# Kernel tuning notes

Hardware: AMD Instinct MI355X
Metric: run time of the kernel (lower is better)

The kernel has to match this reference:

```python
import jax, jax.numpy as jnp
import numpy as np

NEG_SLOPE = 0.2  # both GATConv internal LeakyReLU and the module-level activation


def gat_conv(x, src, dst, W, a_src, a_dst, bias):
    """PyG GATConv (concat=True, add_self_loops handled by caller via src/dst).
    x: [N, Din]; W: [Din, H*C]; a_src, a_dst: [H, C]; bias: [H*C]."""
    N = x.shape[0]
    H, C = a_src.shape
    h = (x @ W).reshape(N, H, C)                       # [N, H, C]
    al_src = jnp.einsum('nhc,hc->nh', h, a_src)        # [N, H]
    al_dst = jnp.einsum('nhc,hc->nh', h, a_dst)        # [N, H]
    e = jax.nn.leaky_relu(al_src[src] + al_dst[dst], NEG_SLOPE)  # [E, H]
    # segment softmax over edges grouped by destination node
    m = jax.ops.segment_max(e, dst, num_segments=N)    # [N, H]
    ex = jnp.exp(e - m[dst])
    denom = jax.ops.segment_sum(ex, dst, num_segments=N)
    alpha = ex / denom[dst]                            # [E, H]
    out = jax.ops.segment_sum(alpha[:, :, None] * h[src], dst, num_segments=N)
    return out.reshape(N, H * C) + bias


def setup_inputs() -> dict:
    key = jax.random.key(0)
    N, E = 50000, 800000
    D_IN, HID, H = 128, 128, 2
    C = HID // H
    ks = jax.random.split(key, 20)
    inp = {
        'x': jax.random.normal(ks[0], (N, D_IN), dtype=jnp.float32),
        'edge_index': jax.random.randint(ks[1], (2, E), 0, N, dtype=jnp.int64),
    }
    dims = [D_IN, HID, HID]  # input dims of the 3 GATConv layers
    for i, din in enumerate(dims, start=1):
        s = 1.0 / np.sqrt(din)
        inp[f'W{i}'] = jax.random.normal(ks[2 + 4 * i], (din, HID), dtype=jnp.float32) * s
        inp[f'a_src{i}'] = jax.random.normal(ks[3 + 4 * i], (H, C), dtype=jnp.float32) * 0.1
        inp[f'a_dst{i}'] = jax.random.normal(ks[4 + 4 * i], (H, C), dtype=jnp.float32) * 0.1
        inp[f'b{i}'] = jnp.zeros((HID,), dtype=jnp.float32)
    inp['lin_w'] = jax.random.normal(ks[2], (HID, 1), dtype=jnp.float32) * (1.0 / np.sqrt(HID))
    inp['lin_b'] = jnp.zeros((1,), dtype=jnp.float32)
    return inp


def reference(x, edge_index, W1, a_src1, a_dst1, b1, W2, a_src2, a_dst2, b2,
              W3, a_src3, a_dst3, b3, lin_w, lin_b):
    N = x.shape[0]
    loops = jnp.arange(N, dtype=edge_index.dtype)
    src = jnp.concatenate([edge_index[0], loops])  # add_self_loops=True
    dst = jnp.concatenate([edge_index[1], loops])

    h = jax.nn.leaky_relu(gat_conv(x, src, dst, W1, a_src1, a_dst1, b1), NEG_SLOPE)
    # dropout is identity in eval mode (p=0.0)
    h = jax.nn.leaky_relu(h + gat_conv(h, src, dst, W2, a_src2, a_dst2, b2), NEG_SLOPE)
    h = jax.nn.leaky_relu(h + gat_conv(h, src, dst, W3, a_src3, a_dst3, b3), NEG_SLOPE)
    logits = (h @ lin_w + lin_b).squeeze(-1)  # [N]
    return logits
```

## Files before the change

kernel.cpp:

```cpp
#include <hip/hip_runtime.h>
#include <hip/hip_bf16.h>
#include <hip/hip_fp16.h>

#define LEAK 0.2f
#define BCAP 4096
#define NTILE 8
#define TSHIFT 13

typedef _Float16 half8  __attribute__((ext_vector_type(8)));
typedef _Float16 half4v __attribute__((ext_vector_type(4)));
typedef float    float4v __attribute__((ext_vector_type(4)));


__global__ __launch_bounds__(256) void k_binscatter(const int* __restrict__ esrc,
                                                    const int* __restrict__ edst,
                                                    int* __restrict__ gcnt,
                                                    unsigned int* __restrict__ binned,
                                                    int E, int ETOT, int NBK, int eb,
                                                    const float* __restrict__ W0,
                                                    const float* __restrict__ W1,
                                                    const float* __restrict__ W2,
                                                    _Float16* __restrict__ w16t) {
    int t = threadIdx.x;
    if (blockIdx.x >= eb) {
        __shared__ _Float16 tile[64][68];
        int bb = blockIdx.x - eb;
        int m = bb >> 2;
        int ti = (bb >> 1) & 1, tj = bb & 1;
        const float* src = (m == 0) ? W0 : (m == 1 ? W1 : W2);
        _Float16* dst = w16t + m * 16384;
        for (int idx = t; idx < 4096; idx += 256) {
            int r = idx >> 6, c = idx & 63;
            tile[r][c] = (_Float16)src[(ti * 64 + r) * 128 + tj * 64 + c];
        }
        __syncthreads();
        for (int idx = t; idx < 4096; idx += 256) {
            int c = idx >> 6, r = idx & 63;
            dst[(tj * 64 + c) * 128 + ti * 64 + r] = tile[r][c];
        }
        return;
    }
    __shared__ int lh[512];
    __shared__ int lbase[512];
    for (int b = t; b < NBK; b += 256) lh[b] = 0;
    __syncthreads();
    int base = blockIdx.x * 4096;
    unsigned int word[16]; int bb[16], rk[16];
    #pragma unroll
    for (int u = 0; u < 16; ++u) {
        int e = base + u * 256 + t;
        bb[u] = -1;
        if (e < ETOT) {
            int s, d;
            if (e < E) { s = esrc[e]; d = edst[e]; } else { s = d = e - E; }
            int b = d >> 7;
            bb[u] = b;
            rk[u] = atomicAdd(&lh[b], 1);
            word[u] = (unsigned int)s | ((unsigned int)(d & 127) << 17);
        }
    }
    __syncthreads();
    for (int b = t; b < NBK; b += 256) {
        int c = lh[b];
        lbase[b] = c ? atomicAdd(&gcnt[b], c) : 0;
    }
    __syncthreads();
    #pragma unroll
    for (int u = 0; u < 16; ++u)
        if (bb[u] >= 0)
            binned[(size_t)bb[u] * BCAP + lbase[bb[u]] + rk[u]] = word[u];
}

__device__ void scatter2_body(int b, const unsigned int* __restrict__ binned,
                              const int* __restrict__ gcnt,
                              int2* __restrict__ offend,
                              int* __restrict__ csr, int N) {
    __shared__ int deg[128 * NTILE];
    __shared__ int lcur[128 * NTILE];
    __shared__ int wt[2];
    int t = threadIdx.x;
    int n0 = b << 7;
    for (int i = t; i < 128 * NTILE; i += 256) deg[i] = 0;
    __syncthreads();
    int beg = b * BCAP, end = beg + gcnt[b];
    for (int i = beg + t; i < end; i += 256) {
        unsigned int u = binned[i];
        atomicAdd(&deg[(u >> 17) * NTILE + ((u & 0x1FFFF) >> TSHIFT)], 1);
    }
    __syncthreads();
    int v = 0, x = 0;
    if (t < 128) {
        #pragma unroll
        for (int k = 0; k < NTILE; ++k) v += deg[t * NTILE + k];
        x = v;
        int lane = t & 63;
        #pragma unroll
        for (int o = 1; o < 64; o <<= 1) {
            int y = __shfl_up(x, o);
            if (lane >= o) x += y;
        }
        if (lane == 63) wt[t >> 6] = x;
    }
    __syncthreads();
    if (t < 128) {
        int excl = x - v + ((t >= 64) ? wt[0] : 0) + beg;
        int run = excl;
        #pragma unroll
        for (int k = 0; k < NTILE; ++k) {
            lcur[t * NTILE + k] = run;
            run += deg[t * NTILE + k];
        }
        int node = n0 + t;
        if (node < N) offend[node] = make_int2(excl, excl + v);
    }
    __syncthreads();
    for (int i = beg + t; i < end; i += 256) {
        unsigned int u = binned[i];
        int pos = atomicAdd(&lcur[(u >> 17) * NTILE + ((u & 0x1FFFF) >> TSHIFT)], 1);
        csr[pos] = (int)(u & 0x1FFFF);
    }
}


__global__ __launch_bounds__(256) void k_gemm_mfma(const void* __restrict__ Xv, int xfp16,
                                                   const _Float16* __restrict__ WhT,
                                                   const float* __restrict__ a_src,
                                                   const float* __restrict__ a_dst,
                                                   _Float16* __restrict__ Hout,
                                                   float* __restrict__ alsrc,
                                                   float* __restrict__ aldst, int N,
                                                   int csr_nb,
                                                   const unsigned int* __restrict__ binned,
                                                   const int* __restrict__ gcnt,
                                                   int2* __restrict__ offend,
                                                   int* __restrict__ csr) {
    if ((int)blockIdx.x < csr_nb) {
        scatter2_body((int)blockIdx.x, binned, gcnt, offend, csr, N);
        return;
    }
    __shared__ _Float16 As[64][136];
    __shared__ float sS[64][2];
    __shared__ float sD[64][2];
    const int t = threadIdx.x;
    const int lane = t & 63, w = t >> 6;
    const int block_row = ((int)blockIdx.x - csr_nb) * 64;

    if (t < 128) { sS[t >> 1][t & 1] = 0.f; sD[t >> 1][t & 1] = 0.f; }

    if (xfp16) {
        const _Float16* Xh = (const _Float16*)Xv;
        #pragma unroll
        for (int it = 0; it < 4; ++it) {
            int i = t + 256 * it;
            int row = i >> 4, c8 = i & 15;
            int gr = block_row + row;
            half8 hv = (half8){0,0,0,0,0,0,0,0};
            if (gr < N) hv = *(const half8*)(Xh + (size_t)gr * 128 + c8 * 8);
            *(half8*)(&As[row][c8 * 8]) = hv;
        }
    } else {
        const float* X = (const float*)Xv;
        #pragma unroll
        for (int it = 0; it < 8; ++it) {
            int i = t + 256 * it;
            int row = i >> 5, c4 = i & 31;
            int gr = block_row + row;
            float4 xv = make_float4(0.f, 0.f, 0.f, 0.f);
            if (gr < N) xv = *(const float4*)(X + (size_t)gr * 128 + c4 * 4);
            half4v hv;
            hv[0] = (_Float16)xv.x; hv[1] = (_Float16)xv.y;
            hv[2] = (_Float16)xv.z; hv[3] = (_Float16)xv.w;
            *(half4v*)(&As[row][c4 * 4]) = hv;
        }
    }

    const int l15 = lane & 15, kq = (lane >> 4) * 8;
    half8 bf[2][4];
    #pragma unroll
    for (int ntl = 0; ntl < 2; ++ntl) {
        int n0 = (w * 2 + ntl) * 16 + l15;
        #pragma unroll
        for (int kt = 0; kt < 4; ++kt)
            bf[ntl][kt] = *(const half8*)(WhT + (size_t)n0 * 128 + kt * 32 + kq);
    }
    __syncthreads();

    float4v acc[4][2];
    #pragma unroll
    for (int mt = 0; mt < 4; ++mt)
        #pragma unroll
        for (int ntl = 0; ntl < 2; ++ntl)
            acc[mt][ntl] = (float4v){0.f, 0.f, 0.f, 0.f};

    #pragma unroll
    for (int kt = 0; kt < 4; ++kt) {
        half8 a[4];
        #pragma unroll
        for (int mt = 0; mt < 4; ++mt)
            a[mt] = *(const half8*)(&As[mt * 16 + l15][kt * 32 + kq]);
        #pragma unroll
        for (int mt = 0; mt < 4; ++mt)
            #pragma unroll
            for (int ntl = 0; ntl < 2; ++ntl)
                acc[mt][ntl] = __builtin_amdgcn_mfma_f32_16x16x32_f16(
                    a[mt], bf[ntl][kt], acc[mt][ntl], 0, 0, 0);
    }

    #pragma unroll
    for (int mt = 0; mt < 4; ++mt) {
        int r0 = block_row + mt * 16 + (lane >> 4) * 4;
        #pragma unroll
        for (int ntl = 0; ntl < 2; ++ntl) {
            int col = (w * 2 + ntl) * 16 + l15;
            #pragma unroll
            for (int reg = 0; reg < 4; ++reg) {
                int r = r0 + reg;
                if (r < N) Hout[(size_t)r * 128 + col] = (_Float16)acc[mt][ntl][reg];
            }
        }
    }

    {
        int c0 = w * 32 + l15, c1 = c0 + 16;
        float as0 = a_src[c0], as1 = a_src[c1];
        float ad0 = a_dst[c0], ad1 = a_dst[c1];
        int head = w >> 1;
        #pragma unroll
        for (int mt = 0; mt < 4; ++mt) {
            #pragma unroll
            for (int reg = 0; reg < 4; ++reg) {
                float ps = (float)acc[mt][0][reg] * as0 + (float)acc[mt][1][reg] * as1;
                float pd = (float)acc[mt][0][reg] * ad0 + (float)acc[mt][1][reg] * ad1;
                #pragma unroll
                for (int o = 1; o < 16; o <<= 1) {
                    ps += __shfl_xor(ps, o);
                    pd += __shfl_xor(pd, o);
                }
                if (l15 == 0) {
                    int row = mt * 16 + (lane >> 4) * 4 + reg;
                    atomicAdd(&sS[row][head], ps);
                    atomicAdd(&sD[row][head], pd);
                }
            }
        }
    }
    __syncthreads();
    if (t < 128) {
        int row = t >> 1, head = t & 1;
        int gr = block_row + row;
        if (gr < N) {
            alsrc[gr * 2 + head] = sS[row][head];
            aldst[gr * 2 + head] = sD[row][head];
        }
    }
}


__global__ __launch_bounds__(256) void k_aggregate(
        const _Float16* __restrict__ H16,
        const float* __restrict__ alsrc,
        const float* __restrict__ aldst,
        const int2* __restrict__ offend,
        const int* __restrict__ csr,
        const float* __restrict__ bias,
        const _Float16* __restrict__ prev,
        _Float16* __restrict__ Out,
        const float* __restrict__ lw, const float* __restrict__ lb,
        float* __restrict__ logits, int N, int mode) {
    int wglobal = (int)((blockIdx.x * 256 + threadIdx.x) >> 6);
    int lane = threadIdx.x & 63;
    if (wglobal * 2 >= N) return;
    int half = lane >> 5;
    int hl = lane & 31;
    int node = wglobal * 2 + half;
    bool active = node < N;
    int nodeC = active ? node : (N - 1);
    int2 oe = offend[nodeC];
    int beg = oe.x;
    int end = active ? oe.y : beg;
    float2 adv = *(const float2*)(aldst + (size_t)nodeC * 2);
    float ad0 = adv.x, ad1 = adv.y;

    int p = hl & 15;
    int q = hl >> 4;
    bool head0 = p < 8;
    const _Float16* hbase = H16 + p * 8;
    int hb = half << 5;

    float acc[8];
    #pragma unroll
    for (int k = 0; k < 8; ++k) acc[k] = 0.f;
    float dsum = 0.f;

    for (int base = beg; base < end; base += 32) {
        int i = base + hl;
        int s = 0; float w0 = 0.f, w1 = 0.f;
        if (i < end) {
            s = csr[i];
            float2 al = *(const float2*)(&alsrc[s * 2]);
            float e0 = al.x + ad0; e0 = e0 > 0.f ? e0 : LEAK * e0;
            float e1 = al.y + ad1; e1 = e1 > 0.f ? e1 : LEAK * e1;
            w0 = __expf(e0); w1 = __expf(e1);
        }
        int cnt = min(32, end - base);
        int iters = (cnt + 1) >> 1;
        int jj = 0;
        for (; jj + 4 <= iters; jj += 4) {
            int sl0 = hb + (jj << 1) + q;
            int sj0 = __shfl(s, sl0), sj1 = __shfl(s, sl0 + 2);
            int sj2 = __shfl(s, sl0 + 4), sj3 = __shfl(s, sl0 + 6);
            float w00 = __shfl(w0, sl0),     w10 = __shfl(w1, sl0);
            float w01 = __shfl(w0, sl0 + 2), w11 = __shfl(w1, sl0 + 2);
            float w02 = __shfl(w0, sl0 + 4), w12 = __shfl(w1, sl0 + 4);
            float w03 = __shfl(w0, sl0 + 6), w13 = __shfl(w1, sl0 + 6);
            float ws0 = head0 ? w00 : w10;
            float ws1 = head0 ? w01 : w11;
            float ws2 = head0 ? w02 : w12;
            float ws3 = head0 ? w03 : w13;
            uint4 r0 = *(const uint4*)(hbase + (size_t)sj0 * 128);
            uint4 r1 = *(const uint4*)(hbase + (size_t)sj1 * 128);
            uint4 r2 = *(const uint4*)(hbase + (size_t)sj2 * 128);
            uint4 r3 = *(const uint4*)(hbase + (size_t)sj3 * 128);
            const _Float16* h0 = (const _Float16*)&r0;
            const _Float16* h1 = (const _Float16*)&r1;
            const _Float16* h2 = (const _Float16*)&r2;
            const _Float16* h3 = (const _Float16*)&r3;
            #pragma unroll
            for (int k = 0; k < 8; ++k) acc[k] += ws0 * (float)h0[k];
            #pragma unroll
            for (int k = 0; k < 8; ++k) acc[k] += ws1 * (float)h1[k];
            #pragma unroll
            for (int k = 0; k < 8; ++k) acc[k] += ws2 * (float)h2[k];
            #pragma unroll
            for (int k = 0; k < 8; ++k) acc[k] += ws3 * (float)h3[k];
            dsum += (ws0 + ws1) + (ws2 + ws3);
        }
        for (; jj + 2 <= iters; jj += 2) {
            int sl0 = hb + (jj << 1) + q;
            int sj0 = __shfl(s, sl0), sj1 = __shfl(s, sl0 + 2);
            float w00 = __shfl(w0, sl0),     w10 = __shfl(w1, sl0);
            float w01 = __shfl(w0, sl0 + 2), w11 = __shfl(w1, sl0 + 2);
            float ws0 = head0 ? w00 : w10;
            float ws1 = head0 ? w01 : w11;
            uint4 r0 = *(const uint4*)(hbase + (size_t)sj0 * 128);
            uint4 r1 = *(const uint4*)(hbase + (size_t)sj1 * 128);
            const _Float16* h0 = (const _Float16*)&r0;
            const _Float16* h1 = (const _Float16*)&r1;
            #pragma unroll
            for (int k = 0; k < 8; ++k) acc[k] += ws0 * (float)h0[k];
            #pragma unroll
            for (int k = 0; k < 8; ++k) acc[k] += ws1 * (float)h1[k];
            dsum += ws0 + ws1;
        }
        if (jj < iters) {
            int sl = hb + (jj << 1) + q;
            int   sj = __shfl(s,  sl);
            float wa = __shfl(w0, sl);
            float wb = __shfl(w1, sl);
            float ws = head0 ? wa : wb;
            uint4 raw = *(const uint4*)(hbase + (size_t)sj * 128);
            const _Float16* h = (const _Float16*)&raw;
            #pragma unroll
            for (int k = 0; k < 8; ++k) acc[k] += ws * (float)h[k];
            dsum += ws;
        }
    }

    #pragma unroll
    for (int k = 0; k < 8; ++k) acc[k] += __shfl_xor(acc[k], 16);
    dsum += __shfl_xor(dsum, 16);

    if (q == 0 && active) {
        float inv = 1.f / dsum;
        int c0 = p * 8;
        float v[8];
        #pragma unroll
        for (int k = 0; k < 8; ++k) v[k] = acc[k] * inv + bias[c0 + k];
        if (mode >= 1) {
            half8 pv = *(const half8*)(prev + (size_t)node * 128 + c0);
            #pragma unroll
            for (int k = 0; k < 8; ++k) v[k] += (float)pv[k];
        }
        #pragma unroll
        for (int k = 0; k < 8; ++k) v[k] = v[k] > 0.f ? v[k] : LEAK * v[k];
        if (mode == 2) {
            float partial = 0.f;
            #pragma unroll
            for (int k = 0; k < 8; ++k) partial += v[k] * lw[c0 + k];
            partial += __shfl_xor(partial, 1);
            partial += __shfl_xor(partial, 2);
            partial += __shfl_xor(partial, 4);
            partial += __shfl_xor(partial, 8);
            if (hl == 0) logits[node] = partial + lb[0];
        } else {
            half8 ov;
            #pragma unroll
            for (int k = 0; k < 8; ++k) ov[k] = (_Float16)v[k];
            *(half8*)(Out + (size_t)node * 128 + c0) = ov;
        }
    }
}


extern "C" void kernel_launch(void* const* d_in, const int* in_sizes, int n_in,
                              void* d_out, int out_size, void* d_ws, size_t ws_size,
                              hipStream_t stream) {
    const float* x    = (const float*)d_in[0];
    const int*   edge = (const int*)d_in[1];
    const float* W[3]  = {(const float*)d_in[2], (const float*)d_in[6], (const float*)d_in[10]};
    const float* as[3] = {(const float*)d_in[3], (const float*)d_in[7], (const float*)d_in[11]};
    const float* ad[3] = {(const float*)d_in[4], (const float*)d_in[8], (const float*)d_in[12]};
    const float* bs[3] = {(const float*)d_in[5], (const float*)d_in[9], (const float*)d_in[13]};
    const float* lw = (const float*)d_in[14];
    const float* lb = (const float*)d_in[15];

    const int N    = in_sizes[0] / 128;
    const int E    = in_sizes[1] / 2;
    const int ETOT = E + N;
    const int NBK  = (N + 127) >> 7;

    char* base = (char*)d_ws;
    size_t o = 0;
    auto carve = [&](size_t bytes) {
        char* p = base + o;
        o = (o + bytes + 255) & ~(size_t)255;
        return p;
    };
    int2*     offend = (int2*)    carve((size_t)N * 8);
    int*      gcnt   = (int*)     carve((size_t)NBK * 4);
    unsigned* binned = (unsigned*)carve((size_t)NBK * BCAP * 4);
    int*      csr    = (int*)     carve((size_t)NBK * BCAP * 4);
    float*    alsrc  = (float*)   carve((size_t)N * 2 * 4);
    float*    aldst  = (float*)   carve((size_t)N * 2 * 4);
    _Float16* h16    = (_Float16*)carve((size_t)N * 128 * 2);
    _Float16* bufA   = (_Float16*)carve((size_t)N * 128 * 2);
    _Float16* bufB   = (_Float16*)carve((size_t)N * 128 * 2);
    _Float16* w16t   = (_Float16*)carve((size_t)3 * 16384 * 2);
    (void)ws_size; (void)n_in; (void)out_size;

    const int* esrc = edge;
    const int* edst = edge + E;

    int eb = (ETOT + 4095) / 4096;

    hipMemsetAsync(gcnt, 0, (size_t)NBK * 4, stream);

    k_binscatter<<<eb + 12, 256, 0, stream>>>(esrc, edst, gcnt, binned, E, ETOT, NBK, eb,
                                              W[0], W[1], W[2], w16t);

    int gemm_blocks = (N + 63) / 64;
    int agg_blocks  = (N + 7) / 8;

    k_gemm_mfma<<<NBK + gemm_blocks, 256, 0, stream>>>(x, 0, w16t, as[0], ad[0], h16,
                                                       alsrc, aldst, N, NBK,
                                                       binned, gcnt, offend, csr);
    k_aggregate<<<agg_blocks, 256, 0, stream>>>(h16, alsrc, aldst, offend, csr,
                                                bs[0], nullptr, bufA, lw, lb, nullptr, N, 0);
    k_gemm_mfma<<<gemm_blocks, 256, 0, stream>>>(bufA, 1, w16t + 16384, as[1], ad[1], h16,
                                                 alsrc, aldst, N, 0,
                                                 binned, gcnt, offend, csr);
    k_aggregate<<<agg_blocks, 256, 0, stream>>>(h16, alsrc, aldst, offend, csr,
                                                bs[1], bufA, bufB, lw, lb, nullptr, N, 1);
    k_gemm_mfma<<<gemm_blocks, 256, 0, stream>>>(bufB, 1, w16t + 32768, as[2], ad[2], h16,
                                                 alsrc, aldst, N, 0,
                                                 binned, gcnt, offend, csr);
    k_aggregate<<<agg_blocks, 256, 0, stream>>>(h16, alsrc, aldst, offend, csr,
                                                bs[2], bufB, nullptr, lw, lb, (float*)d_out, N, 2);
}
```

Baseline: 269.8 us.

## Stage gathered neighbor feature rows into LDS via async global_load_lds

The aggregate kernel now bulk-gathers each chunk's neighbor rows of the fp16 feature matrix straight into LDS using global_load_lds, shared by both nodes in a wave, then reads them back from LDS in the accumulate loops. Blocks shrink to 128 threads with 32 KB of LDS per block. The aim is to issue all gathers up front and overlap their latency instead of serialising per-row register loads. In exchange it adds a full vmcnt(0) wait per chunk and LDS traffic, and the larger LDS footprint may limit occupancy.

```diff
diff --git a/kernel.cpp b/kernel.cpp
--- a/kernel.cpp
+++ b/kernel.cpp
@@ -256,7 +256,7 @@
 }
 
 
-__global__ __launch_bounds__(256) void k_aggregate(
+__global__ __launch_bounds__(128) void k_aggregate(
         const _Float16* __restrict__ H16,
         const float* __restrict__ alsrc,
         const float* __restrict__ aldst,
@@ -267,7 +267,10 @@
         _Float16* __restrict__ Out,
         const float* __restrict__ lw, const float* __restrict__ lb,
         float* __restrict__ logits, int N, int mode) {
-    int wglobal = (int)((blockIdx.x * 256 + threadIdx.x) >> 6);
+    __shared__ uint4 smem[2048];
+    int wave = threadIdx.x >> 6;
+    uint4* wvbase = smem + wave * 1024;
+    int wglobal = (int)((blockIdx.x * 128 + threadIdx.x) >> 6);
     int lane = threadIdx.x & 63;
     if (wglobal * 2 >= N) return;
     int half = lane >> 5;
@@ -284,31 +287,57 @@
     int p = hl & 15;
     int q = hl >> 4;
     bool head0 = p < 8;
-    const _Float16* hbase = H16 + p * 8;
     int hb = half << 5;
+    int g = lane >> 4;
+    int p16 = lane & 15;
+
+    int total = end - beg;
+    int tother = __shfl_xor(total, 32);
+    int maxtot = total > tother ? total : tother;
 
     float acc[8];
     #pragma unroll
     for (int k = 0; k < 8; ++k) acc[k] = 0.f;
     float dsum = 0.f;
 
-    for (int base = beg; base < end; base += 32) {
-        int i = base + hl;
+    for (int cs = 0; cs < maxtot; cs += 32) {
+        int i = beg + cs + hl;
         int s = 0; float w0 = 0.f, w1 = 0.f;
-        if (i < end) {
+        if (cs + hl < total) {
             s = csr[i];
             float2 al = *(const float2*)(&alsrc[s * 2]);
             float e0 = al.x + ad0; e0 = e0 > 0.f ? e0 : LEAK * e0;
             float e1 = al.y + ad1; e1 = e1 > 0.f ? e1 : LEAK * e1;
             w0 = __expf(e0); w1 = __expf(e1);
         }
-        int cnt = min(32, end - base);
-        int iters = (cnt + 1) >> 1;
+        int rem = total - cs;
+        int cntme = rem < 0 ? 0 : (rem > 32 ? 32 : rem);
+        int cntot = __shfl_xor(cntme, 32);
+        int c0 = half ? cntot : cntme;
+        int c1 = half ? cntme : cntot;
+        int nrows = c0 + c1;
+        if (nrows == 0) continue;
+
+        int nr1 = nrows + 1; if (nr1 > 64) nr1 = 64;
+        int nstage = (nr1 + 3) >> 2;
+        for (int k = 0; k < nstage; ++k) {
+            int m = 4 * k + g;
+            int srclane = (m < c0) ? m : (32 + m - c0);
+            srclane &= 63;
+            int sj = __shfl(s, srclane);
+            const _Float16* gp = H16 + (size_t)sj * 128 + p16 * 8;
+            __builtin_amdgcn_global_load_lds(
+                (__attribute__((address_space(1))) const void*)gp,
+                (__attribute__((address_space(3))) void*)(wvbase + k * 64),
+                16, 0, 0);
+        }
+        asm volatile("s_waitcnt vmcnt(0)" ::: "memory");
+
+        const uint4* lrow = wvbase + (size_t)((half ? c0 : 0) + q) * 16 + p;
+        int iters = (cntme + 1) >> 1;
         int jj = 0;
         for (; jj + 4 <= iters; jj += 4) {
             int sl0 = hb + (jj << 1) + q;
-            int sj0 = __shfl(s, sl0), sj1 = __shfl(s, sl0 + 2);
-            int sj2 = __shfl(s, sl0 + 4), sj3 = __shfl(s, sl0 + 6);
             float w00 = __shfl(w0, sl0),     w10 = __shfl(w1, sl0);
             float w01 = __shfl(w0, sl0 + 2), w11 = __shfl(w1, sl0 + 2);
             float w02 = __shfl(w0, sl0 + 4), w12 = __shfl(w1, sl0 + 4);
@@ -317,10 +346,10 @@
             float ws1 = head0 ? w01 : w11;
             float ws2 = head0 ? w02 : w12;
             float ws3 = head0 ? w03 : w13;
-            uint4 r0 = *(const uint4*)(hbase + (size_t)sj0 * 128);
-            uint4 r1 = *(const uint4*)(hbase + (size_t)sj1 * 128);
-            uint4 r2 = *(const uint4*)(hbase + (size_t)sj2 * 128);
-            uint4 r3 = *(const uint4*)(hbase + (size_t)sj3 * 128);
+            uint4 r0 = lrow[(jj + 0) * 32];
+            uint4 r1 = lrow[(jj + 1) * 32];
+            uint4 r2 = lrow[(jj + 2) * 32];
+            uint4 r3 = lrow[(jj + 3) * 32];
             const _Float16* h0 = (const _Float16*)&r0;
             const _Float16* h1 = (const _Float16*)&r1;
             const _Float16* h2 = (const _Float16*)&r2;
@@ -337,13 +366,12 @@
         }
         for (; jj + 2 <= iters; jj += 2) {
             int sl0 = hb + (jj << 1) + q;
-            int sj0 = __shfl(s, sl0), sj1 = __shfl(s, sl0 + 2);
             float w00 = __shfl(w0, sl0),     w10 = __shfl(w1, sl0);
             float w01 = __shfl(w0, sl0 + 2), w11 = __shfl(w1, sl0 + 2);
             float ws0 = head0 ? w00 : w10;
             float ws1 = head0 ? w01 : w11;
-            uint4 r0 = *(const uint4*)(hbase + (size_t)sj0 * 128);
-            uint4 r1 = *(const uint4*)(hbase + (size_t)sj1 * 128);
+            uint4 r0 = lrow[(jj + 0) * 32];
+            uint4 r1 = lrow[(jj + 1) * 32];
             const _Float16* h0 = (const _Float16*)&r0;
             const _Float16* h1 = (const _Float16*)&r1;
             #pragma unroll
@@ -354,11 +382,10 @@
         }
         if (jj < iters) {
             int sl = hb + (jj << 1) + q;
-            int   sj = __shfl(s,  sl);
             float wa = __shfl(w0, sl);
             float wb = __shfl(w1, sl);
             float ws = head0 ? wa : wb;
-            uint4 raw = *(const uint4*)(hbase + (size_t)sj * 128);
+            uint4 raw = lrow[jj * 32];
             const _Float16* h = (const _Float16*)&raw;
             #pragma unroll
             for (int k = 0; k < 8; ++k) acc[k] += ws * (float)h[k];
@@ -449,21 +476,21 @@
                                               W[0], W[1], W[2], w16t);
 
     int gemm_blocks = (N + 63) / 64;
-    int agg_blocks  = (N + 7) / 8;
+    int agg_blocks  = (N + 3) / 4;
 
     k_gemm_mfma<<<NBK + gemm_blocks, 256, 0, stream>>>(x, 0, w16t, as[0], ad[0], h16,
                                                        alsrc, aldst, N, NBK,
                                                        binned, gcnt, offend, csr);
-    k_aggregate<<<agg_blocks, 256, 0, stream>>>(h16, alsrc, aldst, offend, csr,
+    k_aggregate<<<agg_blocks, 128, 0, stream>>>(h16, alsrc, aldst, offend, csr,
                                                 bs[0], nullptr, bufA, lw, lb, nullptr, N, 0);
     k_gemm_mfma<<<gemm_blocks, 256, 0, stream>>>(bufA, 1, w16t + 16384, as[1], ad[1], h16,
                                                  alsrc, aldst, N, 0,
                                                  binned, gcnt, offend, csr);
-    k_aggregate<<<agg_blocks, 256, 0, stream>>>(h16, alsrc, aldst, offend, csr,
+    k_aggregate<<<agg_blocks, 128, 0, stream>>>(h16, alsrc, aldst, offend, csr,
                                                 bs[1], bufA, bufB, lw, lb, nullptr, N, 1);
     k_gemm_mfma<<<gemm_blocks, 256, 0, stream>>>(bufB, 1, w16t + 32768, as[2], ad[2], h16,
                                                  alsrc, aldst, N, 0,
                                                  binned, gcnt, offend, csr);
-    k_aggregate<<<agg_blocks, 256, 0, stream>>>(h16, alsrc, aldst, offend, csr,
+    k_aggregate<<<agg_blocks, 128, 0, stream>>>(h16, alsrc, aldst, offend, csr,
                                                 bs[2], bufB, nullptr, lw, lb, (float*)d_out, N, 2);
 }
```

After: 344.7 us. 1.28x slower.

## Fuse aggregation with next layer's GEMM and attention-logit computation

Applied to the files above, without the earlier changes.

Adds a k_agg_gemm kernel in which each 64-node block aggregates its nodes' neighbour features and writes the activated result to shared memory. It then immediately runs the next layer's MFMA GEMM and the attention-score reductions on that tile. This removes two kernel launches and the global round trip of re-reading the aggregated activations for the GEMM, at the cost of double-buffered h16 and alpha arrays. Aggregation now runs in 64-node blocks (8 nodes per wave), with a sync before the GEMM, which may lower parallelism and latency hiding in the gather phase compared with the separate aggregate kernel.

```diff
diff --git a/kernel.cpp b/kernel.cpp
--- a/kernel.cpp
+++ b/kernel.cpp
@@ -251,6 +251,235 @@
         if (gr < N) {
             alsrc[gr * 2 + head] = sS[row][head];
             aldst[gr * 2 + head] = sD[row][head];
+        }
+    }
+}
+
+
+__global__ __launch_bounds__(256) void k_agg_gemm(
+        const _Float16* __restrict__ H16in,
+        const float* __restrict__ alsrcL,
+        const float* __restrict__ aldstL,
+        const int2* __restrict__ offend,
+        const int* __restrict__ csr,
+        const float* __restrict__ biasL,
+        const _Float16* __restrict__ prev,
+        _Float16* __restrict__ Res,
+        const _Float16* __restrict__ WhT,
+        const float* __restrict__ a_src,
+        const float* __restrict__ a_dst,
+        _Float16* __restrict__ Hout,
+        float* __restrict__ alsrcO,
+        float* __restrict__ aldstO,
+        int N, int mode) {
+    __shared__ _Float16 As[64][136];
+    __shared__ float sS[64][2];
+    __shared__ float sD[64][2];
+    const int t = threadIdx.x;
+    const int lane = t & 63, w = t >> 6;
+    const int block_row = (int)blockIdx.x * 64;
+
+    if (t < 128) { sS[t >> 1][t & 1] = 0.f; sD[t >> 1][t & 1] = 0.f; }
+
+    const int half = lane >> 5;
+    const int hl = lane & 31;
+    const int p = hl & 15;
+    const int q = hl >> 4;
+    const bool head0 = p < 8;
+    const _Float16* hbase = H16in + p * 8;
+    const int hb = half << 5;
+
+    for (int j = 0; j < 8; ++j) {
+        int node = block_row + w * 16 + j * 2 + half;
+        bool active = node < N;
+        int nodeC = active ? node : (N - 1);
+        int2 oe = offend[nodeC];
+        int beg = oe.x;
+        int end = active ? oe.y : beg;
+        float2 adv = *(const float2*)(aldstL + (size_t)nodeC * 2);
+        float ad0 = adv.x, ad1 = adv.y;
+
+        float acc[8];
+        #pragma unroll
+        for (int k = 0; k < 8; ++k) acc[k] = 0.f;
+        float dsum = 0.f;
+
+        for (int base = beg; base < end; base += 32) {
+            int i = base + hl;
+            int s = 0; float w0 = 0.f, w1 = 0.f;
+            if (i < end) {
+                s = csr[i];
+                float2 al = *(const float2*)(&alsrcL[s * 2]);
+                float e0 = al.x + ad0; e0 = e0 > 0.f ? e0 : LEAK * e0;
+                float e1 = al.y + ad1; e1 = e1 > 0.f ? e1 : LEAK * e1;
+                w0 = __expf(e0); w1 = __expf(e1);
+            }
+            int cnt = min(32, end - base);
+            int iters = (cnt + 1) >> 1;
+            int jj = 0;
+            for (; jj + 4 <= iters; jj += 4) {
+                int sl0 = hb + (jj << 1) + q;
+                int sj0 = __shfl(s, sl0), sj1 = __shfl(s, sl0 + 2);
+                int sj2 = __shfl(s, sl0 + 4), sj3 = __shfl(s, sl0 + 6);
+                float w00 = __shfl(w0, sl0),     w10 = __shfl(w1, sl0);
+                float w01 = __shfl(w0, sl0 + 2), w11 = __shfl(w1, sl0 + 2);
+                float w02 = __shfl(w0, sl0 + 4), w12 = __shfl(w1, sl0 + 4);
+                float w03 = __shfl(w0, sl0 + 6), w13 = __shfl(w1, sl0 + 6);
+                float ws0 = head0 ? w00 : w10;
+                float ws1 = head0 ? w01 : w11;
+                float ws2 = head0 ? w02 : w12;
+                float ws3 = head0 ? w03 : w13;
+                uint4 r0 = *(const uint4*)(hbase + (size_t)sj0 * 128);
+                uint4 r1 = *(const uint4*)(hbase + (size_t)sj1 * 128);
+                uint4 r2 = *(const uint4*)(hbase + (size_t)sj2 * 128);
+                uint4 r3 = *(const uint4*)(hbase + (size_t)sj3 * 128);
+                const _Float16* h0 = (const _Float16*)&r0;
+                const _Float16* h1 = (const _Float16*)&r1;
+                const _Float16* h2 = (const _Float16*)&r2;
+                const _Float16* h3 = (const _Float16*)&r3;
+                #pragma unroll
+                for (int k = 0; k < 8; ++k) acc[k] += ws0 * (float)h0[k];
+                #pragma unroll
+                for (int k = 0; k < 8; ++k) acc[k] += ws1 * (float)h1[k];
+                #pragma unroll
+                for (int k = 0; k < 8; ++k) acc[k] += ws2 * (float)h2[k];
+                #pragma unroll
+                for (int k = 0; k < 8; ++k) acc[k] += ws3 * (float)h3[k];
+                dsum += (ws0 + ws1) + (ws2 + ws3);
+            }
+            for (; jj + 2 <= iters; jj += 2) {
+                int sl0 = hb + (jj << 1) + q;
+                int sj0 = __shfl(s, sl0), sj1 = __shfl(s, sl0 + 2);
+                float w00 = __shfl(w0, sl0),     w10 = __shfl(w1, sl0);
+                float w01 = __shfl(w0, sl0 + 2), w11 = __shfl(w1, sl0 + 2);
+                float ws0 = head0 ? w00 : w10;
+                float ws1 = head0 ? w01 : w11;
+                uint4 r0 = *(const uint4*)(hbase + (size_t)sj0 * 128);
+                uint4 r1 = *(const uint4*)(hbase + (size_t)sj1 * 128);
+                const _Float16* h0 = (const _Float16*)&r0;
+                const _Float16* h1 = (const _Float16*)&r1;
+                #pragma unroll
+                for (int k = 0; k < 8; ++k) acc[k] += ws0 * (float)h0[k];
+                #pragma unroll
+                for (int k = 0; k < 8; ++k) acc[k] += ws1 * (float)h1[k];
+                dsum += ws0 + ws1;
+            }
+            if (jj < iters) {
+                int sl = hb + (jj << 1) + q;
+                int   sj = __shfl(s,  sl);
+                float wa = __shfl(w0, sl);
+                float wb = __shfl(w1, sl);
+                float ws = head0 ? wa : wb;
+                uint4 raw = *(const uint4*)(hbase + (size_t)sj * 128);
+                const _Float16* h = (const _Float16*)&raw;
+                #pragma unroll
+                for (int k = 0; k < 8; ++k) acc[k] += ws * (float)h[k];
+                dsum += ws;
+            }
+        }
+
+        #pragma unroll
+        for (int k = 0; k < 8; ++k) acc[k] += __shfl_xor(acc[k], 16);
+        dsum += __shfl_xor(dsum, 16);
+
+        if (q == 0 && active) {
+            float inv = 1.f / dsum;
+            int c0 = p * 8;
+            float v[8];
+            #pragma unroll
+            for (int k = 0; k < 8; ++k) v[k] = acc[k] * inv + biasL[c0 + k];
+            if (mode >= 1) {
+                half8 pv = *(const half8*)(prev + (size_t)node * 128 + c0);
+                #pragma unroll
+                for (int k = 0; k < 8; ++k) v[k] += (float)pv[k];
+            }
+            #pragma unroll
+            for (int k = 0; k < 8; ++k) v[k] = v[k] > 0.f ? v[k] : LEAK * v[k];
+            half8 ov;
+            #pragma unroll
+            for (int k = 0; k < 8; ++k) ov[k] = (_Float16)v[k];
+            *(half8*)(&As[node - block_row][c0]) = ov;
+            *(half8*)(Res + (size_t)node * 128 + c0) = ov;
+        }
+    }
+    __syncthreads();
+
+    const int l15 = lane & 15, kq = (lane >> 4) * 8;
+    half8 bf[2][4];
+    #pragma unroll
+    for (int ntl = 0; ntl < 2; ++ntl) {
+        int n0 = (w * 2 + ntl) * 16 + l15;
+        #pragma unroll
+        for (int kt = 0; kt < 4; ++kt)
+            bf[ntl][kt] = *(const half8*)(WhT + (size_t)n0 * 128 + kt * 32 + kq);
+    }
+
+    float4v accB[4][2];
+    #pragma unroll
+    for (int mt = 0; mt < 4; ++mt)
+        #pragma unroll
+        for (int ntl = 0; ntl < 2; ++ntl)
+            accB[mt][ntl] = (float4v){0.f, 0.f, 0.f, 0.f};
+
+    #pragma unroll
+    for (int kt = 0; kt < 4; ++kt) {
+        half8 a[4];
+        #pragma unroll
+        for (int mt = 0; mt < 4; ++mt)
+            a[mt] = *(const half8*)(&As[mt * 16 + l15][kt * 32 + kq]);
+        #pragma unroll
+        for (int mt = 0; mt < 4; ++mt)
+            #pragma unroll
+            for (int ntl = 0; ntl < 2; ++ntl)
+                accB[mt][ntl] = __builtin_amdgcn_mfma_f32_16x16x32_f16(
+                    a[mt], bf[ntl][kt], accB[mt][ntl], 0, 0, 0);
+    }
+
+    #pragma unroll
+    for (int mt = 0; mt < 4; ++mt) {
+        int r0 = block_row + mt * 16 + (lane >> 4) * 4;
+        #pragma unroll
+        for (int ntl = 0; ntl < 2; ++ntl) {
+            int col = (w * 2 + ntl) * 16 + l15;
+            #pragma unroll
+            for (int reg = 0; reg < 4; ++reg) {
+                int r = r0 + reg;
+                if (r < N) Hout[(size_t)r * 128 + col] = (_Float16)accB[mt][ntl][reg];
+            }
+        }
+    }
+
+    {
+        int c0 = w * 32 + l15, c1 = c0 + 16;
+        float as0 = a_src[c0], as1 = a_src[c1];
+        float ad0 = a_dst[c0], ad1 = a_dst[c1];
+        int head = w >> 1;
+        #pragma unroll
+        for (int mt = 0; mt < 4; ++mt) {
+            #pragma unroll
+            for (int reg = 0; reg < 4; ++reg) {
+                float ps = (float)accB[mt][0][reg] * as0 + (float)accB[mt][1][reg] * as1;
+                float pd = (float)accB[mt][0][reg] * ad0 + (float)accB[mt][1][reg] * ad1;
+                #pragma unroll
+                for (int o = 1; o < 16; o <<= 1) {
+                    ps += __shfl_xor(ps, o);
+                    pd += __shfl_xor(pd, o);
+                }
+                if (l15 == 0) {
+                    int row = mt * 16 + (lane >> 4) * 4 + reg;
+                    atomicAdd(&sS[row][head], ps);
+                    atomicAdd(&sD[row][head], pd);
+                }
+            }
+        }
+    }
+    __syncthreads();
+    if (t < 128) {
+        int row = t >> 1, head = t & 1;
+        int gr = block_row + row;
+        if (gr < N) {
+            alsrcO[gr * 2 + head] = sS[row][head];
+            aldstO[gr * 2 + head] = sD[row][head];
         }
     }
 }
@@ -430,9 +659,12 @@
     int*      gcnt   = (int*)     carve((size_t)NBK * 4);
     unsigned* binned = (unsigned*)carve((size_t)NBK * BCAP * 4);
     int*      csr    = (int*)     carve((size_t)NBK * BCAP * 4);
-    float*    alsrc  = (float*)   carve((size_t)N * 2 * 4);
-    float*    aldst  = (float*)   carve((size_t)N * 2 * 4);
-    _Float16* h16    = (_Float16*)carve((size_t)N * 128 * 2);
+    float*    alsA   = (float*)   carve((size_t)N * 2 * 4);
+    float*    aldA   = (float*)   carve((size_t)N * 2 * 4);
+    float*    alsB   = (float*)   carve((size_t)N * 2 * 4);
+    float*    aldB   = (float*)   carve((size_t)N * 2 * 4);
+    _Float16* h16a   = (_Float16*)carve((size_t)N * 128 * 2);
+    _Float16* h16b   = (_Float16*)carve((size_t)N * 128 * 2);
     _Float16* bufA   = (_Float16*)carve((size_t)N * 128 * 2);
     _Float16* bufB   = (_Float16*)carve((size_t)N * 128 * 2);
     _Float16* w16t   = (_Float16*)carve((size_t)3 * 16384 * 2);
@@ -451,19 +683,18 @@
     int gemm_blocks = (N + 63) / 64;
     int agg_blocks  = (N + 7) / 8;
 
-    k_gemm_mfma<<<NBK + gemm_blocks, 256, 0, stream>>>(x, 0, w16t, as[0], ad[0], h16,
-                                                       alsrc, aldst, N, NBK,
+    k_gemm_mfma<<<NBK + gemm_blocks, 256, 0, stream>>>(x, 0, w16t, as[0], ad[0], h16a,
+                                                       alsA, aldA, N, NBK,
                                                        binned, gcnt, offend, csr);
-    k_aggregate<<<agg_blocks, 256, 0, stream>>>(h16, alsrc, aldst, offend, csr,
-                                                bs[0], nullptr, bufA, lw, lb, nullptr, N, 0);
-    k_gemm_mfma<<<gemm_blocks, 256, 0, stream>>>(bufA, 1, w16t + 16384, as[1], ad[1], h16,
-                                                 alsrc, aldst, N, 0,
-                                                 binned, gcnt, offend, csr);
-    k_aggregate<<<agg_blocks, 256, 0, stream>>>(h16, alsrc, aldst, offend, csr,
-                                                bs[1], bufA, bufB, lw, lb, nullptr, N, 1);
-    k_gemm_mfma<<<gemm_blocks, 256, 0, stream>>>(bufB, 1, w16t + 32768, as[2], ad[2], h16,
-                                                 alsrc, aldst, N, 0,
-                                                 binned, gcnt, offend, csr);
-    k_aggregate<<<agg_blocks, 256, 0, stream>>>(h16, alsrc, aldst, offend, csr,
-                                                bs[2], bufB, nullptr, lw, lb, (float*)d_out, N, 2);
+    k_agg_gemm<<<gemm_blocks, 256, 0, stream>>>(h16a, alsA, aldA, offend, csr,
+                                                bs[0], nullptr, bufA,
+                                                w16t + 16384, as[1], ad[1],
+                                                h16b, alsB, aldB, N, 0);
+    k_agg_gemm<<<gemm_blocks, 256, 0, stream>>>(h16b, alsB, aldB, offend, csr,
+                                                bs[1], bufA, bufB,
+                                                w16t + 32768, as[2], ad[2],
+                                                h16a, alsA, aldA, N, 1);
+    k_aggregate<<<agg_blocks, 256, 0, stream>>>(h16a, alsA, aldA, offend, csr,
+                                                bs[2], bufB, nullptr, lw, lb,
+                                                (float*)d_out, N, 2);
 }
```

Result: no change. 264.5 us (-1.9%).

## Split aggregation by attention head with XCD-aware block mapping

Applied to the files above, without the earlier changes.

The aggregation kernel now gives each block a single attention head. The head and a node subgroup come from the block ID's low three bits, so each XCD works on one head's 64-column half of H16, which should improve L2 locality on the multi-die GPU. Each 16-lane group handles one node for one head, so the two-head shuffle-and-select logic goes away. The final linear layer now combines the two heads' partial logits with atomicAdd, which needs logits zeroed beforehand; that zeroing is done inside the binscatter kernel. The cost is twice as many node visits, each with its own edge-list and CSR reads, plus atomics on the output.

```diff
diff --git a/kernel.cpp b/kernel.cpp
--- a/kernel.cpp
+++ b/kernel.cpp
@@ -20,7 +20,8 @@
                                                     const float* __restrict__ W0,
                                                     const float* __restrict__ W1,
                                                     const float* __restrict__ W2,
-                                                    _Float16* __restrict__ w16t) {
+                                                    _Float16* __restrict__ w16t,
+                                                    float* __restrict__ logits, int N) {
     int t = threadIdx.x;
     if (blockIdx.x >= eb) {
         __shared__ _Float16 tile[64][68];
@@ -38,6 +39,7 @@
             int c = idx >> 6, r = idx & 63;
             dst[(tj * 64 + c) * 128 + ti * 64 + r] = tile[r][c];
         }
+        for (int i = bb * 256 + t; i < N; i += 12 * 256) logits[i] = 0.f;
         return;
     }
     __shared__ int lh[512];
@@ -256,7 +258,7 @@
 }
 
 
-__global__ __launch_bounds__(256) void k_aggregate(
+__global__ __launch_bounds__(256) void k_aggregate_hs(
         const _Float16* __restrict__ H16,
         const float* __restrict__ alsrc,
         const float* __restrict__ aldst,
@@ -267,56 +269,50 @@
         _Float16* __restrict__ Out,
         const float* __restrict__ lw, const float* __restrict__ lb,
         float* __restrict__ logits, int N, int mode) {
-    int wglobal = (int)((blockIdx.x * 256 + threadIdx.x) >> 6);
-    int lane = threadIdx.x & 63;
-    if (wglobal * 2 >= N) return;
-    int half = lane >> 5;
-    int hl = lane & 31;
-    int node = wglobal * 2 + half;
+    int bid = (int)blockIdx.x;
+    int xcd = bid & 7, g = bid >> 3;
+    int head = xcd >> 2, sub = xcd & 3;
+    int t = threadIdx.x;
+    int w = t >> 6, lane = t & 63;
+    int n4 = lane >> 4;
+    int hl = lane & 15;
+    int p = hl & 7;
+    int q = hl >> 3;
+    int gb = n4 << 4;
+
+    int node = (g * 4 + sub) * 16 + w * 4 + n4;
     bool active = node < N;
     int nodeC = active ? node : (N - 1);
     int2 oe = offend[nodeC];
     int beg = oe.x;
     int end = active ? oe.y : beg;
-    float2 adv = *(const float2*)(aldst + (size_t)nodeC * 2);
-    float ad0 = adv.x, ad1 = adv.y;
-
-    int p = hl & 15;
-    int q = hl >> 4;
-    bool head0 = p < 8;
-    const _Float16* hbase = H16 + p * 8;
-    int hb = half << 5;
+    float adH = aldst[(size_t)nodeC * 2 + head];
+    const _Float16* hbase = H16 + head * 64 + p * 8;
 
     float acc[8];
     #pragma unroll
     for (int k = 0; k < 8; ++k) acc[k] = 0.f;
     float dsum = 0.f;
-
-    for (int base = beg; base < end; base += 32) {
-        int i = base + hl;
-        int s = 0; float w0 = 0.f, w1 = 0.f;
-        if (i < end) {
+    int total = end - beg;
+
+    for (int cs = 0; cs < total; cs += 16) {
+        int i = beg + cs + hl;
+        int s = 0; float wgt = 0.f;
+        if (cs + hl < total) {
             s = csr[i];
-            float2 al = *(const float2*)(&alsrc[s * 2]);
-            float e0 = al.x + ad0; e0 = e0 > 0.f ? e0 : LEAK * e0;
-            float e1 = al.y + ad1; e1 = e1 > 0.f ? e1 : LEAK * e1;
-            w0 = __expf(e0); w1 = __expf(e1);
-        }
-        int cnt = min(32, end - base);
+            float e = alsrc[(size_t)s * 2 + head] + adH;
+            e = e > 0.f ? e : LEAK * e;
+            wgt = __expf(e);
+        }
+        int cnt = min(16, total - cs);
         int iters = (cnt + 1) >> 1;
         int jj = 0;
         for (; jj + 4 <= iters; jj += 4) {
-            int sl0 = hb + (jj << 1) + q;
-            int sj0 = __shfl(s, sl0), sj1 = __shfl(s, sl0 + 2);
+            int sl0 = gb + (jj << 1) + q;
+            int sj0 = __shfl(s, sl0),     sj1 = __shfl(s, sl0 + 2);
             int sj2 = __shfl(s, sl0 + 4), sj3 = __shfl(s, sl0 + 6);
-            float w00 = __shfl(w0, sl0),     w10 = __shfl(w1, sl0);
-            float w01 = __shfl(w0, sl0 + 2), w11 = __shfl(w1, sl0 + 2);
-            float w02 = __shfl(w0, sl0 + 4), w12 = __shfl(w1, sl0 + 4);
-            float w03 = __shfl(w0, sl0 + 6), w13 = __shfl(w1, sl0 + 6);
-            float ws0 = head0 ? w00 : w10;
-            float ws1 = head0 ? w01 : w11;
-            float ws2 = head0 ? w02 : w12;
-            float ws3 = head0 ? w03 : w13;
+            float ws0 = __shfl(wgt, sl0),     ws1 = __shfl(wgt, sl0 + 2);
+            float ws2 = __shfl(wgt, sl0 + 4), ws3 = __shfl(wgt, sl0 + 6);
             uint4 r0 = *(const uint4*)(hbase + (size_t)sj0 * 128);
             uint4 r1 = *(const uint4*)(hbase + (size_t)sj1 * 128);
             uint4 r2 = *(const uint4*)(hbase + (size_t)sj2 * 128);
@@ -336,12 +332,9 @@
             dsum += (ws0 + ws1) + (ws2 + ws3);
         }
         for (; jj + 2 <= iters; jj += 2) {
-            int sl0 = hb + (jj << 1) + q;
+            int sl0 = gb + (jj << 1) + q;
             int sj0 = __shfl(s, sl0), sj1 = __shfl(s, sl0 + 2);
-            float w00 = __shfl(w0, sl0),     w10 = __shfl(w1, sl0);
-            float w01 = __shfl(w0, sl0 + 2), w11 = __shfl(w1, sl0 + 2);
-            float ws0 = head0 ? w00 : w10;
-            float ws1 = head0 ? w01 : w11;
+            float ws0 = __shfl(wgt, sl0), ws1 = __shfl(wgt, sl0 + 2);
             uint4 r0 = *(const uint4*)(hbase + (size_t)sj0 * 128);
             uint4 r1 = *(const uint4*)(hbase + (size_t)sj1 * 128);
             const _Float16* h0 = (const _Float16*)&r0;
@@ -353,11 +346,9 @@
             dsum += ws0 + ws1;
         }
         if (jj < iters) {
-            int sl = hb + (jj << 1) + q;
-            int   sj = __shfl(s,  sl);
-            float wa = __shfl(w0, sl);
-            float wb = __shfl(w1, sl);
-            float ws = head0 ? wa : wb;
+            int sl = gb + (jj << 1) + q;
+            int   sj = __shfl(s,   sl);
+            float ws = __shfl(wgt, sl);
             uint4 raw = *(const uint4*)(hbase + (size_t)sj * 128);
             const _Float16* h = (const _Float16*)&raw;
             #pragma unroll
@@ -367,12 +358,12 @@
     }
 
     #pragma unroll
-    for (int k = 0; k < 8; ++k) acc[k] += __shfl_xor(acc[k], 16);
-    dsum += __shfl_xor(dsum, 16);
+    for (int k = 0; k < 8; ++k) acc[k] += __shfl_xor(acc[k], 8);
+    dsum += __shfl_xor(dsum, 8);
 
     if (q == 0 && active) {
         float inv = 1.f / dsum;
-        int c0 = p * 8;
+        int c0 = head * 64 + p * 8;
         float v[8];
         #pragma unroll
         for (int k = 0; k < 8; ++k) v[k] = acc[k] * inv + bias[c0 + k];
@@ -390,8 +381,8 @@
             partial += __shfl_xor(partial, 1);
             partial += __shfl_xor(partial, 2);
             partial += __shfl_xor(partial, 4);
-            partial += __shfl_xor(partial, 8);
-            if (hl == 0) logits[node] = partial + lb[0];
+            if (p == 0)
+                atomicAdd(&logits[node], partial + (head == 0 ? lb[0] : 0.f));
         } else {
             half8 ov;
             #pragma unroll
@@ -446,24 +437,27 @@
     hipMemsetAsync(gcnt, 0, (size_t)NBK * 4, stream);
 
     k_binscatter<<<eb + 12, 256, 0, stream>>>(esrc, edst, gcnt, binned, E, ETOT, NBK, eb,
-                                              W[0], W[1], W[2], w16t);
+                                              W[0], W[1], W[2], w16t, (float*)d_out, N);
 
     int gemm_blocks = (N + 63) / 64;
-    int agg_blocks  = (N + 7) / 8;
+    int agg_grid = (((N + 15) / 16 + 3) / 4) * 8;
 
     k_gemm_mfma<<<NBK + gemm_blocks, 256, 0, stream>>>(x, 0, w16t, as[0], ad[0], h16,
                                                        alsrc, aldst, N, NBK,
                                                        binned, gcnt, offend, csr);
-    k_aggregate<<<agg_blocks, 256, 0, stream>>>(h16, alsrc, aldst, offend, csr,
-                                                bs[0], nullptr, bufA, lw, lb, nullptr, N, 0);
+    k_aggregate_hs<<<agg_grid, 256, 0, stream>>>(h16, alsrc, aldst, offend, csr,
+                                                 bs[0], nullptr, bufA, lw, lb,
+                                                 nullptr, N, 0);
     k_gemm_mfma<<<gemm_blocks, 256, 0, stream>>>(bufA, 1, w16t + 16384, as[1], ad[1], h16,
                                                  alsrc, aldst, N, 0,
                                                  binned, gcnt, offend, csr);
-    k_aggregate<<<agg_blocks, 256, 0, stream>>>(h16, alsrc, aldst, offend, csr,
-                                                bs[1], bufA, bufB, lw, lb, nullptr, N, 1);
+    k_aggregate_hs<<<agg_grid, 256, 0, stream>>>(h16, alsrc, aldst, offend, csr,
+                                                 bs[1], bufA, bufB, lw, lb,
+                                                 nullptr, N, 1);
     k_gemm_mfma<<<gemm_blocks, 256, 0, stream>>>(bufB, 1, w16t + 32768, as[2], ad[2], h16,
                                                  alsrc, aldst, N, 0,
                                                  binned, gcnt, offend, csr);
-    k_aggregate<<<agg_blocks, 256, 0, stream>>>(h16, alsrc, aldst, offend, csr,
-                                                bs[2], bufB, nullptr, lw, lb, (float*)d_out, N, 2);
+    k_aggregate_hs<<<agg_grid, 256, 0, stream>>>(h16, alsrc, aldst, offend, csr,
+                                                 bs[2], bufB, nullptr, lw, lb,
+                                                 (float*)d_out, N, 2);
 }
```

Result: no change. 266.5 us (-1.2%).
